# Kernel optimization log

Measured on AMD Instinct MI355X. Metric: run time of the kernel, lower is better.

## Reference

```python
import jax, jax.numpy as jnp
import numpy as np

NUM_HEADS = 12
EPS = 1e-12  # torch F.normalize clamp_min eps


def _l2norm(t):
    return t / jnp.clip(jnp.linalg.norm(t, axis=-1, keepdims=True), EPS)


def setup_inputs() -> dict:
    key = jax.random.key(0)
    ks = jax.random.split(key, 6)
    B, N, C = 8, 4096, 768
    Nc, Nb, F = 1, 512, 16
    s = 0.02
    return {
        "x": jax.random.normal(ks[0], (B, N, C), jnp.float32),
        "bank": jax.random.normal(ks[1], (Nc, Nb, F), jnp.float32),
        "Wq": jax.random.normal(ks[2], (C, C), jnp.float32) * s,
        "Wkv": jax.random.normal(ks[3], (F, 2 * C), jnp.float32) * s,
        "Wlin": jax.random.normal(ks[4], (C, C), jnp.float32) * s,
        "b_lin": jnp.zeros((C,), jnp.float32),
        "prelu_a": jnp.asarray(0.25, jnp.float32),
        "temperature": jnp.ones((NUM_HEADS, 1, 1), jnp.float32),
    }


def reference(x, bank, Wq, Wkv, Wlin, b_lin, prelu_a, temperature):
    B, N, C = x.shape
    Nc, Nb, _ = bank.shape
    H = NUM_HEADS
    d = C // H
    # q: (B, H, N, d), L2-normalized along d
    q = _l2norm((x @ Wq).reshape(B, N, H, d).transpose(0, 2, 1, 3))
    # kv from (detached) bank: (2, Nc, H, Nb, d)
    kv = (bank @ Wkv).reshape(Nc, Nb, 2, H, d).transpose(2, 0, 3, 1, 4)
    k = _l2norm(kv[0])
    v = kv[1]
    # cosine attention with per-head learned temperature: (B, Nc, H, N, Nb)
    attn = jnp.einsum('bhnd,chmd->bchnm', q, k) * temperature
    attn = jax.nn.softmax(attn, axis=-1)
    # (dropout is identity in eval mode)
    out = jnp.einsum('bchnm,chmd->bchnd', attn, v)  # (B, Nc, H, N, d)
    out = out.reshape(B * Nc, H, N, d).transpose(0, 2, 1, 3).reshape(B, N, C)
    out = out @ Wlin + b_lin
    # PReLU with a single shared parameter
    return jnp.where(out >= 0, out, prelu_a * out)
```

## Files before the change

### kernel.cpp

```cpp
#include <hip/hip_runtime.h>
#include <cstdint>
#include <cstddef>

typedef unsigned short u16;
typedef __attribute__((ext_vector_type(8))) __bf16 bf16x8;
typedef __attribute__((ext_vector_type(4))) float f32x4;

#define MFMA(a, b, c) __builtin_amdgcn_mfma_f32_16x16x32_bf16(a, b, c, 0, 0, 0)

__device__ __forceinline__ u16 f2bf(float f) {
  union { float f; uint32_t u; } x; x.f = f;
  uint32_t r = x.u + 0x7fffu + ((x.u >> 16) & 1u);
  return (u16)(r >> 16);
}

__device__ __forceinline__ void gld16(const u16* g, u16* l) {
  __builtin_amdgcn_global_load_lds(
      (const __attribute__((address_space(1))) void*)g,
      (__attribute__((address_space(3))) void*)l, 16, 0, 0);
}

__global__ void cvt_f32_bf16(const float* __restrict__ src, u16* __restrict__ dst, int n4) {
  int i = blockIdx.x * blockDim.x + threadIdx.x;
  int stride = gridDim.x * blockDim.x;
  for (; i < n4; i += stride) {
    float4 v = ((const float4*)src)[i];
    ushort4 o;
    o.x = f2bf(v.x); o.y = f2bf(v.y); o.z = f2bf(v.z); o.w = f2bf(v.w);
    ((ushort4*)dst)[i] = o;
  }
}

__global__ void transpose_cvt(const float* __restrict__ src, u16* __restrict__ dst, int R, int C) {
  __shared__ float tile[32][33];
  int bx = blockIdx.x * 32, by = blockIdx.y * 32;
  int tx = threadIdx.x, ty = threadIdx.y;
  #pragma unroll
  for (int i = ty; i < 32; i += 8)
    tile[i][tx] = src[(size_t)(by + i) * C + bx + tx];
  __syncthreads();
  #pragma unroll
  for (int i = ty; i < 32; i += 8)
    dst[(size_t)(bx + i) * R + by + tx] = f2bf(tile[tx][i]);
}

__global__ void kv_prep(const float* __restrict__ bank, const float* __restrict__ Wkv,
                        const float* __restrict__ temp, u16* __restrict__ K, u16* __restrict__ VT) {
  int m = blockIdx.x & 511, h = blockIdx.x >> 9;
  int j = threadIdx.x;
  const float* br = bank + m * 16;
  float kj = 0.f, vj = 0.f;
  #pragma unroll
  for (int f = 0; f < 16; ++f) {
    float bv = br[f];
    kj = fmaf(bv, Wkv[f * 1536 + h * 64 + j], kj);
    vj = fmaf(bv, Wkv[f * 1536 + 768 + h * 64 + j], vj);
  }
  float ss = kj * kj;
  #pragma unroll
  for (int o = 32; o; o >>= 1) ss += __shfl_xor(ss, o);
  float rn = rsqrtf(fmaxf(ss, 1e-24f));
  K[((size_t)h * 512 + m) * 64 + j] = f2bf(kj * rn * temp[h] * 1.4426950408889634f);
  VT[((size_t)h * 64 + j) * 512 + m] = f2bf(vj);
}

template <int MODE>
__global__ __launch_bounds__(256, 3) void gemm_bt(
    const u16* __restrict__ A, const u16* __restrict__ BT, void* __restrict__ Cout,
    int M, int N, int K, const float* __restrict__ bias, const float* __restrict__ prelu) {
  __shared__ u16 sA[128 * 32];
  __shared__ u16 sB[128 * 32];
  const int ntiles = N >> 7;
  const int m0 = (blockIdx.x / ntiles) << 7;
  const int n0 = (blockIdx.x % ntiles) << 7;
  const int tid = threadIdx.x;
  const int w = tid >> 6, lane = tid & 63;
  const int wm = (w >> 1) << 6, wn = (w & 1) << 6;
  const int srow = lane >> 2, scol = (lane & 3) << 3;
  const u16* ga = A + (size_t)(m0 + (w << 5) + srow) * K + scol;
  const u16* gb = BT + (size_t)(n0 + (w << 5) + srow) * K + scol;
  u16* la = sA + (w << 5) * 32;
  u16* lb = sB + (w << 5) * 32;
  const int fr = lane & 15, fq = (lane >> 4) << 3;
  f32x4 acc[4][4] = {};

  for (int k0 = 0; k0 < K; k0 += 32) {
    __syncthreads();
    gld16(ga + k0, la);
    gld16(ga + k0 + (size_t)16 * K, la + 16 * 32);
    gld16(gb + k0, lb);
    gld16(gb + k0 + (size_t)16 * K, lb + 16 * 32);
    __syncthreads();
    bf16x8 af[4], bfr[4];
    #pragma unroll
    for (int t = 0; t < 4; ++t) {
      af[t] = *(const bf16x8*)(sA + (wm + t * 16 + fr) * 32 + fq);
      bfr[t] = *(const bf16x8*)(sB + (wn + t * 16 + fr) * 32 + fq);
    }
    #pragma unroll
    for (int i = 0; i < 4; ++i)
      #pragma unroll
      for (int j = 0; j < 4; ++j)
        acc[i][j] = MFMA(af[i], bfr[j], acc[i][j]);
  }

  const int q = lane >> 4;
  float a = (MODE == 1) ? prelu[0] : 0.f;
  #pragma unroll
  for (int tm = 0; tm < 4; ++tm)
    #pragma unroll
    for (int tn = 0; tn < 4; ++tn) {
      int col = n0 + wn + tn * 16 + fr;
      float bv = (MODE == 1) ? bias[col] : 0.f;
      #pragma unroll
      for (int r = 0; r < 4; ++r) {
        int row = m0 + wm + tm * 16 + q * 4 + r;
        float v = acc[tm][tn][r];
        if (MODE == 1) {
          v += bv;
          v = v >= 0.f ? v : v * a;
          ((float*)Cout)[(size_t)row * N + col] = v;
        } else {
          ((u16*)Cout)[(size_t)row * N + col] = f2bf(v);
        }
      }
    }
}

__global__ __launch_bounds__(256, 2) void attn_kern(
    const u16* __restrict__ Q, const u16* __restrict__ Kb,
    const u16* __restrict__ Vt, u16* __restrict__ O) {
  __shared__ __align__(16) u16 sK[2][64 * 72];
  __shared__ __align__(16) u16 sV[2][64 * 72];
  __shared__ __align__(16) u16 pb_s[4][64 * 40];

  const int qb = blockIdx.x & 127;
  const int h = blockIdx.x >> 7;
  const int tid = threadIdx.x, w = tid >> 6, lane = tid & 63;
  const int fr = lane & 15, quad = lane >> 4;
  const int rowbase = qb * 256 + (w << 6);

  bf16x8 qa[4][2];
  #pragma unroll
  for (int g = 0; g < 4; ++g) {
    const u16* qp = Q + (size_t)(rowbase + g * 16 + fr) * 768 + h * 64 + (quad << 3);
    qa[g][0] = *(const bf16x8*)qp;
    qa[g][1] = *(const bf16x8*)(qp + 32);
    float ss = 0.f;
    #pragma unroll
    for (int j = 0; j < 8; ++j) {
      float f0 = (float)qa[g][0][j], f1 = (float)qa[g][1][j];
      ss += f0 * f0 + f1 * f1;
    }
    ss += __shfl_xor(ss, 16);
    ss += __shfl_xor(ss, 32);
    float rn = rsqrtf(fmaxf(ss, 1e-24f));
    #pragma unroll
    for (int j = 0; j < 8; ++j) {
      qa[g][0][j] = (__bf16)((float)qa[g][0][j] * rn);
      qa[g][1][j] = (__bf16)((float)qa[g][1][j] * rn);
    }
  }

  const u16* kg = Kb + (size_t)h * 512 * 64;
  const u16* vg = Vt + (size_t)h * 64 * 512;
  int4 kreg[2], vreg[2];
  auto load_chunk = [&](int c) {
    #pragma unroll
    for (int r = 0; r < 2; ++r) {
      int u = r * 256 + tid;
      kreg[r] = *(const int4*)(kg + (size_t)(c * 64 + (u >> 3)) * 64 + (u & 7) * 8);
      vreg[r] = *(const int4*)(vg + (size_t)(u >> 3) * 512 + c * 64 + (u & 7) * 8);
    }
  };
  auto store_chunk = [&](int buf) {
    #pragma unroll
    for (int r = 0; r < 2; ++r) {
      int u = r * 256 + tid;
      *(int4*)(sK[buf] + (u >> 3) * 72 + (u & 7) * 8) = kreg[r];
      *(int4*)(sV[buf] + (u >> 3) * 72 + (u & 7) * 8) = vreg[r];
    }
  };

  load_chunk(0);
  store_chunk(0);
  load_chunk(1);
  __syncthreads();

  f32x4 oa[4][4] = {};
  float ls[4] = {0.f, 0.f, 0.f, 0.f};
  u16* pw = pb_s[w];

  for (int c = 0; c < 8; ++c) {
    const int cb = c & 1;
    if (c < 7) store_chunk((c + 1) & 1);
    if (c < 6) load_chunk(c + 2);

    f32x4 s[4][4];
    #pragma unroll
    for (int mt = 0; mt < 4; ++mt) {
      const u16* kp = sK[cb] + (mt * 16 + fr) * 72 + (quad << 3);
      bf16x8 ak0 = *(const bf16x8*)kp;
      bf16x8 ak1 = *(const bf16x8*)(kp + 32);
      #pragma unroll
      for (int g = 0; g < 4; ++g) {
        f32x4 z = {0.f, 0.f, 0.f, 0.f};
        z = MFMA(ak0, qa[g][0], z);
        z = MFMA(ak1, qa[g][1], z);
        s[g][mt] = z;
      }
    }
    #pragma unroll
    for (int g = 0; g < 4; ++g)
      #pragma unroll
      for (int mt = 0; mt < 4; ++mt)
        #pragma unroll
        for (int r = 0; r < 4; ++r) {
          float p = __builtin_amdgcn_exp2f(s[g][mt][r]);
          ls[g] += p;
          s[g][mt][r] = p;
        }
    #pragma unroll
    for (int ks = 0; ks < 2; ++ks) {
      #pragma unroll
      for (int g = 0; g < 4; ++g)
        #pragma unroll
        for (int i = 0; i < 2; ++i) {
          f32x4 v = s[g][ks * 2 + i];
          uint32_t lo = (uint32_t)f2bf(v[0]) | ((uint32_t)f2bf(v[1]) << 16);
          uint32_t hi = (uint32_t)f2bf(v[2]) | ((uint32_t)f2bf(v[3]) << 16);
          uint2 pk = {lo, hi};
          *(uint2*)(pw + (g * 16 + fr) * 40 + i * 16 + (quad << 2)) = pk;
        }
      bf16x8 va[4], pbf[4];
      #pragma unroll
      for (int t = 0; t < 4; ++t)
        va[t] = *(const bf16x8*)(sV[cb] + (t * 16 + fr) * 72 + ks * 32 + (quad << 3));
      #pragma unroll
      for (int g = 0; g < 4; ++g)
        pbf[g] = *(const bf16x8*)(pw + (g * 16 + fr) * 40 + (quad << 3));
      #pragma unroll
      for (int g = 0; g < 4; ++g)
        #pragma unroll
        for (int t = 0; t < 4; ++t)
          oa[g][t] = MFMA(va[t], pbf[g], oa[g][t]);
    }
    __syncthreads();
  }

  #pragma unroll
  for (int g = 0; g < 4; ++g) {
    float l = ls[g];
    l += __shfl_xor(l, 16);
    l += __shfl_xor(l, 32);
    float rl = __builtin_amdgcn_rcpf(l);
    u16* op = O + (size_t)(rowbase + g * 16 + fr) * 768 + h * 64 + (quad << 2);
    #pragma unroll
    for (int t = 0; t < 4; ++t) {
      ushort4 pk;
      pk.x = f2bf(oa[g][t][0] * rl);
      pk.y = f2bf(oa[g][t][1] * rl);
      pk.z = f2bf(oa[g][t][2] * rl);
      pk.w = f2bf(oa[g][t][3] * rl);
      *(ushort4*)(op + t * 16) = pk;
    }
  }
}

extern "C" void kernel_launch(void* const* d_in, const int* in_sizes, int n_in,
                              void* d_out, int out_size, void* d_ws, size_t ws_size,
                              hipStream_t stream) {
  const float* x      = (const float*)d_in[0];
  const float* bank   = (const float*)d_in[1];
  const float* Wq     = (const float*)d_in[2];
  const float* Wkv    = (const float*)d_in[3];
  const float* Wlin   = (const float*)d_in[4];
  const float* b_lin  = (const float*)d_in[5];
  const float* prelu  = (const float*)d_in[6];
  const float* temp   = (const float*)d_in[7];
  float* out = (float*)d_out;

  char* ws = (char*)d_ws;
  const size_t NELEM = 25165824;
  u16* qbuf  = (u16*)ws;
  u16* xbuf  = (u16*)(ws + 50331648);
  u16* obuf  = xbuf;
  u16* wqt   = (u16*)(ws + 100663296);
  u16* wlt   = wqt + 589824;
  u16* kbuf  = wlt + 589824;
  u16* vtbuf = kbuf + 393216;

  cvt_f32_bf16<<<4096, 256, 0, stream>>>(x, xbuf, (int)(NELEM / 4));
  transpose_cvt<<<dim3(24, 24), dim3(32, 8), 0, stream>>>(Wq, wqt, 768, 768);
  transpose_cvt<<<dim3(24, 24), dim3(32, 8), 0, stream>>>(Wlin, wlt, 768, 768);
  kv_prep<<<6144, 64, 0, stream>>>(bank, Wkv, temp, kbuf, vtbuf);
  gemm_bt<0><<<1536, 256, 0, stream>>>(xbuf, wqt, qbuf, 32768, 768, 768, nullptr, nullptr);
  attn_kern<<<1536, 256, 0, stream>>>(qbuf, kbuf, vtbuf, obuf);
  gemm_bt<1><<<1536, 256, 0, stream>>>(obuf, wlt, out, 32768, 768, 768, b_lin, prelu);
}
```

Before: 421.7 us.

## Load K/V MFMA fragments directly from global into registers, drop LDS staging

The attention kernel no longer stages K and V tiles through shared memory with block-wide barriers. Each wave loads its MFMA operand fragments for 32-key slices straight from global (L2-resident) memory into registers and double-buffers them across two fragment sets, so the per-chunk __syncthreads disappears. The bf16 conversion of probabilities is simplified to round-half-up plus a byte permute. The trade is redundant global loads across the four waves and more register pressure, plus slightly different rounding of the probabilities.

```diff
diff --git a/kernel.cpp b/kernel.cpp
--- a/kernel.cpp
+++ b/kernel.cpp
@@ -127,11 +127,11 @@
     }
 }
 
+struct KVFrag { bf16x8 k[2][2]; bf16x8 v[4]; };
+
 __global__ __launch_bounds__(256, 2) void attn_kern(
     const u16* __restrict__ Q, const u16* __restrict__ Kb,
     const u16* __restrict__ Vt, u16* __restrict__ O) {
-  __shared__ __align__(16) u16 sK[2][64 * 72];
-  __shared__ __align__(16) u16 sV[2][64 * 72];
   __shared__ __align__(16) u16 pb_s[4][64 * 40];
 
   const int qb = blockIdx.x & 127;
@@ -164,88 +164,67 @@
 
   const u16* kg = Kb + (size_t)h * 512 * 64;
   const u16* vg = Vt + (size_t)h * 64 * 512;
-  int4 kreg[2], vreg[2];
-  auto load_chunk = [&](int c) {
-    #pragma unroll
-    for (int r = 0; r < 2; ++r) {
-      int u = r * 256 + tid;
-      kreg[r] = *(const int4*)(kg + (size_t)(c * 64 + (u >> 3)) * 64 + (u & 7) * 8);
-      vreg[r] = *(const int4*)(vg + (size_t)(u >> 3) * 512 + c * 64 + (u & 7) * 8);
-    }
+
+  auto load_kv = [&](KVFrag& f, int s) {
+    const u16* kp = kg + (size_t)(s * 32 + fr) * 64 + (quad << 3);
+    f.k[0][0] = *(const bf16x8*)kp;
+    f.k[0][1] = *(const bf16x8*)(kp + 32);
+    f.k[1][0] = *(const bf16x8*)(kp + 16 * 64);
+    f.k[1][1] = *(const bf16x8*)(kp + 16 * 64 + 32);
+    const u16* vp = vg + (size_t)fr * 512 + s * 32 + (quad << 3);
+    #pragma unroll
+    for (int t = 0; t < 4; ++t)
+      f.v[t] = *(const bf16x8*)(vp + (size_t)t * 16 * 512);
   };
-  auto store_chunk = [&](int buf) {
-    #pragma unroll
-    for (int r = 0; r < 2; ++r) {
-      int u = r * 256 + tid;
-      *(int4*)(sK[buf] + (u >> 3) * 72 + (u & 7) * 8) = kreg[r];
-      *(int4*)(sV[buf] + (u >> 3) * 72 + (u & 7) * 8) = vreg[r];
-    }
-  };
-
-  load_chunk(0);
-  store_chunk(0);
-  load_chunk(1);
-  __syncthreads();
 
   f32x4 oa[4][4] = {};
   float ls[4] = {0.f, 0.f, 0.f, 0.f};
   u16* pw = pb_s[w];
 
-  for (int c = 0; c < 8; ++c) {
-    const int cb = c & 1;
-    if (c < 7) store_chunk((c + 1) & 1);
-    if (c < 6) load_chunk(c + 2);
-
-    f32x4 s[4][4];
-    #pragma unroll
-    for (int mt = 0; mt < 4; ++mt) {
-      const u16* kp = sK[cb] + (mt * 16 + fr) * 72 + (quad << 3);
-      bf16x8 ak0 = *(const bf16x8*)kp;
-      bf16x8 ak1 = *(const bf16x8*)(kp + 32);
+  auto compute = [&](KVFrag& f) {
+    f32x4 sc[4][2];
+    #pragma unroll
+    for (int mt = 0; mt < 2; ++mt)
       #pragma unroll
       for (int g = 0; g < 4; ++g) {
         f32x4 z = {0.f, 0.f, 0.f, 0.f};
-        z = MFMA(ak0, qa[g][0], z);
-        z = MFMA(ak1, qa[g][1], z);
-        s[g][mt] = z;
+        z = MFMA(f.k[mt][0], qa[g][0], z);
+        z = MFMA(f.k[mt][1], qa[g][1], z);
+        sc[g][mt] = z;
       }
-    }
     #pragma unroll
     for (int g = 0; g < 4; ++g)
       #pragma unroll
-      for (int mt = 0; mt < 4; ++mt)
+      for (int mt = 0; mt < 2; ++mt) {
+        uint32_t u[4];
         #pragma unroll
         for (int r = 0; r < 4; ++r) {
-          float p = __builtin_amdgcn_exp2f(s[g][mt][r]);
+          float p = __builtin_amdgcn_exp2f(sc[g][mt][r]);
           ls[g] += p;
-          s[g][mt][r] = p;
+          u[r] = __builtin_bit_cast(uint32_t, p) + 0x8000u;
         }
-    #pragma unroll
-    for (int ks = 0; ks < 2; ++ks) {
-      #pragma unroll
-      for (int g = 0; g < 4; ++g)
-        #pragma unroll
-        for (int i = 0; i < 2; ++i) {
-          f32x4 v = s[g][ks * 2 + i];
-          uint32_t lo = (uint32_t)f2bf(v[0]) | ((uint32_t)f2bf(v[1]) << 16);
-          uint32_t hi = (uint32_t)f2bf(v[2]) | ((uint32_t)f2bf(v[3]) << 16);
-          uint2 pk = {lo, hi};
-          *(uint2*)(pw + (g * 16 + fr) * 40 + i * 16 + (quad << 2)) = pk;
-        }
-      bf16x8 va[4], pbf[4];
+        uint2 pk;
+        pk.x = __builtin_amdgcn_perm(u[1], u[0], 0x07060302);
+        pk.y = __builtin_amdgcn_perm(u[3], u[2], 0x07060302);
+        *(uint2*)(pw + (g * 16 + fr) * 40 + mt * 16 + (quad << 2)) = pk;
+      }
+    #pragma unroll
+    for (int g = 0; g < 4; ++g) {
+      bf16x8 pbf = *(const bf16x8*)(pw + (g * 16 + fr) * 40 + (quad << 3));
       #pragma unroll
       for (int t = 0; t < 4; ++t)
-        va[t] = *(const bf16x8*)(sV[cb] + (t * 16 + fr) * 72 + ks * 32 + (quad << 3));
-      #pragma unroll
-      for (int g = 0; g < 4; ++g)
-        pbf[g] = *(const bf16x8*)(pw + (g * 16 + fr) * 40 + (quad << 3));
-      #pragma unroll
-      for (int g = 0; g < 4; ++g)
-        #pragma unroll
-        for (int t = 0; t < 4; ++t)
-          oa[g][t] = MFMA(va[t], pbf[g], oa[g][t]);
-    }
-    __syncthreads();
+        oa[g][t] = MFMA(f.v[t], pbf, oa[g][t]);
+    }
+  };
+
+  KVFrag fA, fB;
+  load_kv(fA, 0);
+  load_kv(fB, 1);
+  for (int it = 0; it < 8; ++it) {
+    compute(fA);
+    if (it < 7) load_kv(fA, 2 * it + 2);
+    compute(fB);
+    if (it < 7) load_kv(fB, 2 * it + 3);
   }
 
   #pragma unroll
```

Result: slower. 437.5 us (+3.8%).
